# Optimization experiments

Measured on AMD Instinct MI355X. Metric: run time of the kernel, lower is better.

## Reference

```python
import jax, jax.numpy as jnp
from jax import lax
import numpy as np

B, C_IN, C_OUT, RN, H, W = 8, 64, 64, 4, 128, 128
DN = ('NCHW', 'OIHW', 'NCHW')
BN_EPS = 1e-5


def setup_inputs() -> dict:
    key = jax.random.key(0)
    k1, k2, k3, k4 = jax.random.split(key, 4)
    x = jax.random.normal(k1, (B, C_IN, H, W), dtype=jnp.float32)
    # per-sample, per-region dynamic 3x3 kernels (generated by a hypernet upstream)
    kernel = jax.random.normal(k2, (B, RN, C_OUT, C_IN, 3, 3), dtype=jnp.float32) * 0.05
    mask_w = jax.random.normal(k3, (RN, C_IN, 3, 3), dtype=jnp.float32) * 0.05
    mask_b = jax.random.normal(k4, (RN,), dtype=jnp.float32) * 0.01
    bn_gamma = jnp.ones((C_OUT,), dtype=jnp.float32)
    bn_beta = jnp.zeros((C_OUT,), dtype=jnp.float32)
    bn_mean = jnp.zeros((C_OUT,), dtype=jnp.float32)
    bn_var = jnp.ones((C_OUT,), dtype=jnp.float32)
    return {"x": x, "kernel": kernel, "mask_w": mask_w, "mask_b": mask_b,
            "bn_gamma": bn_gamma, "bn_beta": bn_beta,
            "bn_mean": bn_mean, "bn_var": bn_var}


def reference(x, kernel, mask_w, mask_b, bn_gamma, bn_beta, bn_mean, bn_var):
    b, c, h, w = x.shape
    rn, out_c = kernel.shape[1], kernel.shape[2]

    # region masks: 3x3 conv -> softmax over region axis (eval path of GumbelSoftmax2D)
    logits = lax.conv_general_dilated(x, mask_w, (1, 1), 'SAME', dimension_numbers=DN)
    logits = logits + mask_b[None, :, None, None]          # [b, RN, h, w]
    masks = jax.nn.softmax(logits, axis=1)

    # per-sample per-region dynamic conv as one grouped conv with b*RN groups
    xg = jnp.broadcast_to(x[:, None], (b, rn, c, h, w)).reshape(1, b * rn * c, h, w)
    kg = kernel.reshape(b * rn * out_c, c, 3, 3)
    y = lax.conv_general_dilated(xg, kg, (1, 1), 'SAME', dimension_numbers=DN,
                                 feature_group_count=b * rn)
    y = y.reshape(b, rn, out_c, h, w)

    # mask-weighted sum over regions
    y = jnp.sum(y * masks[:, :, None], axis=1)             # [b, out_c, h, w]

    # BatchNorm2d (eval: running stats) + ReLU
    inv = bn_gamma / jnp.sqrt(bn_var + BN_EPS)
    y = (y - bn_mean[None, :, None, None]) * inv[None, :, None, None] \
        + bn_beta[None, :, None, None]
    out = jax.nn.relu(y)
    return out, masks
```

## Files before the change

### kernel.cpp

```cpp
#include <hip/hip_runtime.h>
#include <hip/hip_bf16.h>

#define B_    8
#define CIN   64
#define COUT  64
#define RN_   4
#define H_    128
#define W_    128
#define HW_   (H_ * W_)
#define BN_EPS 1e-5f

typedef short v8s __attribute__((ext_vector_type(8)));
typedef float v4f __attribute__((ext_vector_type(4)));

__device__ __forceinline__ unsigned short f2bf(float f) {
    unsigned int u = __float_as_uint(f);
    u += 0x7FFFu + ((u >> 16) & 1u);
    return (unsigned short)(u >> 16);
}

__global__ __launch_bounds__(256) void prep(const float* __restrict__ x,
                                            const float* __restrict__ kr,
                                            unsigned short* __restrict__ xT,
                                            unsigned short* __restrict__ kT) {
    __shared__ float sl[16 * 64 * 9];
    if (blockIdx.x < 1024) {
        const int b = blockIdx.x >> 7, h = blockIdx.x & 127;
        const float* xp = x + (size_t)b * CIN * HW_ + (size_t)h * W_;
        for (int idx = threadIdx.x; idx < CIN * W_; idx += 256) {
            const int c = idx >> 7, w = idx & 127;
            sl[c * 129 + w] = xp[(size_t)c * HW_ + w];
        }
        __syncthreads();
        unsigned short* op = xT + ((size_t)b * H_ + h) * (W_ * CIN);
        for (int idx = threadIdx.x; idx < (W_ * CIN) / 8; idx += 256) {
            const int w = idx >> 3, c0 = (idx & 7) << 3;
            int4 v;
            v.x = f2bf(sl[(c0 + 0) * 129 + w]) | ((unsigned)f2bf(sl[(c0 + 1) * 129 + w]) << 16);
            v.y = f2bf(sl[(c0 + 2) * 129 + w]) | ((unsigned)f2bf(sl[(c0 + 3) * 129 + w]) << 16);
            v.z = f2bf(sl[(c0 + 4) * 129 + w]) | ((unsigned)f2bf(sl[(c0 + 5) * 129 + w]) << 16);
            v.w = f2bf(sl[(c0 + 6) * 129 + w]) | ((unsigned)f2bf(sl[(c0 + 7) * 129 + w]) << 16);
            *(int4*)(op + (w << 6) + c0) = v;
        }
    } else {
        const int bid = blockIdx.x - 1024;
        const int br = bid >> 2, oq = bid & 3;
        const float* src = kr + ((size_t)br * 64 + oq * 16) * (64 * 9);
        for (int idx = threadIdx.x; idx < 2304; idx += 256)
            *(float4*)&sl[idx << 2] = *(const float4*)&src[idx << 2];
        __syncthreads();
        unsigned short* dst = kT + (size_t)br * (9 * 4096) + oq * (16 * 64);
        for (int idx = threadIdx.x; idx < 1152; idx += 256) {
            const int t = idx >> 7, rem = idx & 127, o16 = rem >> 3, c8 = (rem & 7) << 3;
            unsigned short s[8];
            #pragma unroll
            for (int j = 0; j < 8; j++)
                s[j] = f2bf(sl[(o16 * 64 + c8 + j) * 9 + t]);
            int4 v;
            v.x = s[0] | ((unsigned)s[1] << 16);
            v.y = s[2] | ((unsigned)s[3] << 16);
            v.z = s[4] | ((unsigned)s[5] << 16);
            v.w = s[6] | ((unsigned)s[7] << 16);
            *(int4*)(dst + t * 4096 + o16 * 64 + c8) = v;
        }
    }
}

#define WPAD     72
#define XS_W     66
#define XS_ROWS  6
#define AS_ELEMS (COUT * WPAD)
#define XS_ELEMS (XS_ROWS * XS_W * WPAD)

__global__ __launch_bounds__(256, 2) void main_conv(
        const unsigned short* __restrict__ xT,
        const unsigned short* __restrict__ kT,
        const float* __restrict__ mw, const float* __restrict__ mb,
        const float* __restrict__ bn_gamma, const float* __restrict__ bn_beta,
        const float* __restrict__ bn_mean,  const float* __restrict__ bn_var,
        float* __restrict__ outp, float* __restrict__ masks_g) {
    __shared__ unsigned short xs[XS_ELEMS];
    __shared__ unsigned short as[2 * AS_ELEMS];
    __shared__ unsigned short mws[9 * 4 * 64];
    __shared__ float scale_s[COUT];
    __shared__ float shift_s[COUT];

    const int tid = threadIdx.x;
    const int b  = blockIdx.z;
    const int w0 = blockIdx.y << 6;
    const int h0 = blockIdx.x << 2;
    const int lane = tid & 63, wv = tid >> 6;
    const int i = lane & 15, g = lane >> 4;
    const int h_out = h0 + wv;

    const unsigned short* kb = kT + (size_t)b * (36 * 4096);
    int4 areg[2];
    #pragma unroll
    for (int q = 0; q < 2; q++)
        areg[q] = *(const int4*)(kb + ((q * 256 + tid) << 3));

    const unsigned short* xb = xT + (size_t)b * (HW_ * CIN);
    #pragma unroll
    for (int row = 0; row < XS_ROWS; row++) {
        const int h_in = h0 - 1 + row;
        const bool hok = (h_in >= 0) && (h_in < H_);
        for (int idx = tid; idx < XS_W * 8; idx += 256) {
            const int w = idx >> 3, c8 = (idx & 7) << 3;
            const int w_in = w0 - 1 + w;
            int4 v = make_int4(0, 0, 0, 0);
            if (hok && (w_in >= 0) && (w_in < W_))
                v = *(const int4*)(xb + ((h_in * W_ + w_in) << 6) + c8);
            *(int4*)(&xs[(row * XS_W + w) * WPAD + c8]) = v;
        }
    }
    for (int idx = tid; idx < 9 * 4 * 64; idx += 256) {
        const int t = idx >> 8, rc = idx & 255, r = rc >> 6, c = rc & 63;
        mws[(t << 8) + (r << 6) + c] = f2bf(mw[((r << 6) + c) * 9 + t]);
    }
    if (tid < COUT) {
        const float sc = bn_gamma[tid] * rsqrtf(bn_var[tid] + BN_EPS);
        scale_s[tid] = sc;
        shift_s[tid] = bn_beta[tid] - bn_mean[tid] * sc;
    }
    const float mb0 = mb[0], mb1 = mb[1], mb2 = mb[2], mb3 = mb[3];

    int bbase[4];
    #pragma unroll
    for (int fn = 0; fn < 4; fn++)
        bbase[fn] = ((wv + 1) * XS_W + fn * 16 + i + 1) * WPAD + g * 8;

    v4f y_acc[4][4], o_acc[4][4], lg_acc[4];
    #pragma unroll
    for (int fm = 0; fm < 4; fm++)
        #pragma unroll
        for (int fn = 0; fn < 4; fn++) {
            y_acc[fm][fn] = (v4f){0.f, 0.f, 0.f, 0.f};
            o_acc[fm][fn] = (v4f){0.f, 0.f, 0.f, 0.f};
        }
    #pragma unroll
    for (int fn = 0; fn < 4; fn++) lg_acc[fn] = (v4f){0.f, 0.f, 0.f, 0.f};

    unsigned mk0[4], mk1[4];

    int r = 0, tap = 0;
    for (int rt = 0; rt < 36; rt++) {
        const int buf = (rt & 1) * AS_ELEMS;
        #pragma unroll
        for (int q = 0; q < 2; q++) {
            const int c = q * 256 + tid;
            *(int4*)(&as[buf + (c >> 3) * WPAD + ((c & 7) << 3)]) = areg[q];
        }
        __syncthreads();
        if (rt < 35) {
            const unsigned short* kn = kb + ((rt + 1) << 12);
            #pragma unroll
            for (int q = 0; q < 2; q++)
                areg[q] = *(const int4*)(kn + ((q * 256 + tid) << 3));
        }
        const int toff = ((tap / 3) * XS_W + (tap % 3)) * WPAD - (XS_W + 1) * WPAD;
        const bool do_lg = (rt < 9);
        #pragma unroll
        for (int ks = 0; ks < 2; ks++) {
            v8s a[4], bfr[4];
            #pragma unroll
            for (int fm = 0; fm < 4; fm++)
                a[fm] = *(const v8s*)(&as[buf + (fm * 16 + i) * WPAD + ks * 32 + g * 8]);
            #pragma unroll
            for (int fn = 0; fn < 4; fn++)
                bfr[fn] = *(const v8s*)(&xs[bbase[fn] + toff + ks * 32]);
            if (do_lg) {
                const v8s am = *(const v8s*)(&mws[(tap << 8) + ((i & 3) << 6) + ks * 32 + g * 8]);
                #pragma unroll
                for (int fn = 0; fn < 4; fn++)
                    lg_acc[fn] = __builtin_amdgcn_mfma_f32_16x16x32_bf16(
                        am, bfr[fn], lg_acc[fn], 0, 0, 0);
            }
            #pragma unroll
            for (int fm = 0; fm < 4; fm++)
                #pragma unroll
                for (int fn = 0; fn < 4; fn++)
                    y_acc[fm][fn] = __builtin_amdgcn_mfma_f32_16x16x32_bf16(
                        a[fm], bfr[fn], y_acc[fm][fn], 0, 0, 0);
        }
        if (rt == 8) {
            #pragma unroll
            for (int fn = 0; fn < 4; fn++) {
                const float l0 = lg_acc[fn][0] + mb0, l1 = lg_acc[fn][1] + mb1;
                const float l2 = lg_acc[fn][2] + mb2, l3 = lg_acc[fn][3] + mb3;
                const float mx = fmaxf(fmaxf(l0, l1), fmaxf(l2, l3));
                const float e0 = __expf(l0 - mx), e1 = __expf(l1 - mx);
                const float e2 = __expf(l2 - mx), e3 = __expf(l3 - mx);
                const float inv = 1.f / (e0 + e1 + e2 + e3);
                const float m0 = e0 * inv, m1 = e1 * inv, m2 = e2 * inv, m3 = e3 * inv;
                if (g == 0) {
                    float* mp = masks_g + ((size_t)b * RN_ * H_ + h_out) * W_ + w0 + fn * 16 + i;
                    mp[0] = m0; mp[HW_] = m1; mp[2 * HW_] = m2; mp[3 * HW_] = m3;
                }
                mk0[fn] = f2bf(m0) | ((unsigned)f2bf(m1) << 16);
                mk1[fn] = f2bf(m2) | ((unsigned)f2bf(m3) << 16);
            }
        }
        if (++tap == 9) {
            tap = 0;
            #pragma unroll
            for (int fn = 0; fn < 4; fn++) {
                unsigned pk = (r & 2) ? mk1[fn] : mk0[fn];
                pk = __shfl(pk, i);
                const float mv = (r & 1) ? __uint_as_float(pk & 0xffff0000u)
                                         : __uint_as_float(pk << 16);
                #pragma unroll
                for (int fm = 0; fm < 4; fm++) {
                    o_acc[fm][fn] += mv * y_acc[fm][fn];
                    y_acc[fm][fn] = (v4f){0.f, 0.f, 0.f, 0.f};
                }
            }
            r++;
        }
    }

    #pragma unroll
    for (int fm = 0; fm < 4; fm++) {
        #pragma unroll
        for (int reg = 0; reg < 4; reg++) {
            const int o = fm * 16 + g * 4 + reg;
            const float sc = scale_s[o], sh = shift_s[o];
            float* rowp = outp + (((size_t)b * COUT + o) * H_ + h_out) * W_ + w0 + i;
            #pragma unroll
            for (int fn = 0; fn < 4; fn++) {
                const float v = o_acc[fm][fn][reg] * sc + sh;
                rowp[fn * 16] = fmaxf(v, 0.f);
            }
        }
    }
}

extern "C" void kernel_launch(void* const* d_in, const int* in_sizes, int n_in,
                              void* d_out, int out_size, void* d_ws, size_t ws_size,
                              hipStream_t stream) {
    const float* x     = (const float*)d_in[0];
    const float* kr    = (const float*)d_in[1];
    const float* mw    = (const float*)d_in[2];
    const float* mb    = (const float*)d_in[3];
    const float* gamma = (const float*)d_in[4];
    const float* beta  = (const float*)d_in[5];
    const float* mean  = (const float*)d_in[6];
    const float* var   = (const float*)d_in[7];

    float* outp  = (float*)d_out;
    float* masks = outp + (size_t)B_ * COUT * HW_;

    unsigned short* xT = (unsigned short*)d_ws;
    unsigned short* kT = xT + (size_t)B_ * HW_ * CIN;

    hipLaunchKernelGGL(prep, dim3(1152), dim3(256), 0, stream, x, kr, xT, kT);
    hipLaunchKernelGGL(main_conv, dim3(H_ / 4, 2, B_), dim3(256), 0, stream,
                       xT, kT, mw, mb, gamma, beta, mean, var, outp, masks);
}
```

Measured before the change: 156.5 us.

## Load dynamic-kernel A fragments directly from global into registers, unroll tap loop

Removes the shared-memory staging buffer for the per-sample weight tiles. Each lane now loads its MFMA A fragments straight from global memory into a double-buffered register array, which drops the per-step __syncthreads and the LDS writes and reads. The 36-step loop is fully unrolled with compile-time tap offsets. The cost is higher register pressure (16 v8s fragments) and redundant global loads across waves, since all four waves fetch the same weights.

```diff
diff --git a/kernel.cpp b/kernel.cpp
--- a/kernel.cpp
+++ b/kernel.cpp
@@ -69,7 +69,6 @@
 #define WPAD     72
 #define XS_W     66
 #define XS_ROWS  6
-#define AS_ELEMS (COUT * WPAD)
 #define XS_ELEMS (XS_ROWS * XS_W * WPAD)
 
 __global__ __launch_bounds__(256, 2) void main_conv(
@@ -80,7 +79,6 @@
         const float* __restrict__ bn_mean,  const float* __restrict__ bn_var,
         float* __restrict__ outp, float* __restrict__ masks_g) {
     __shared__ unsigned short xs[XS_ELEMS];
-    __shared__ unsigned short as[2 * AS_ELEMS];
     __shared__ unsigned short mws[9 * 4 * 64];
     __shared__ float scale_s[COUT];
     __shared__ float shift_s[COUT];
@@ -93,11 +91,12 @@
     const int i = lane & 15, g = lane >> 4;
     const int h_out = h0 + wv;
 
-    const unsigned short* kb = kT + (size_t)b * (36 * 4096);
-    int4 areg[2];
-    #pragma unroll
-    for (int q = 0; q < 2; q++)
-        areg[q] = *(const int4*)(kb + ((q * 256 + tid) << 3));
+    const unsigned short* ka = kT + (size_t)b * (36 * 4096) + (i << 6) + (g << 3);
+
+    v8s ab[2][8];
+    #pragma unroll
+    for (int f = 0; f < 8; f++)
+        ab[0][f] = *(const v8s*)(ka + ((f >> 1) << 10) + ((f & 1) << 5));
 
     const unsigned short* xb = xT + (size_t)b * (HW_ * CIN);
     #pragma unroll
@@ -127,7 +126,7 @@
     int bbase[4];
     #pragma unroll
     for (int fn = 0; fn < 4; fn++)
-        bbase[fn] = ((wv + 1) * XS_W + fn * 16 + i + 1) * WPAD + g * 8;
+        bbase[fn] = (wv * XS_W + fn * 16 + i) * WPAD + g * 8;
 
     v4f y_acc[4][4], o_acc[4][4], lg_acc[4];
     #pragma unroll
@@ -142,81 +141,83 @@
 
     unsigned mk0[4], mk1[4];
 
-    int r = 0, tap = 0;
-    for (int rt = 0; rt < 36; rt++) {
-        const int buf = (rt & 1) * AS_ELEMS;
-        #pragma unroll
-        for (int q = 0; q < 2; q++) {
-            const int c = q * 256 + tid;
-            *(int4*)(&as[buf + (c >> 3) * WPAD + ((c & 7) << 3)]) = areg[q];
-        }
-        __syncthreads();
-        if (rt < 35) {
-            const unsigned short* kn = kb + ((rt + 1) << 12);
+    auto do_softmax = [&]() {
+        #pragma unroll
+        for (int fn = 0; fn < 4; fn++) {
+            const float l0 = lg_acc[fn][0] + mb0, l1 = lg_acc[fn][1] + mb1;
+            const float l2 = lg_acc[fn][2] + mb2, l3 = lg_acc[fn][3] + mb3;
+            const float mx = fmaxf(fmaxf(l0, l1), fmaxf(l2, l3));
+            const float e0 = __expf(l0 - mx), e1 = __expf(l1 - mx);
+            const float e2 = __expf(l2 - mx), e3 = __expf(l3 - mx);
+            const float inv = 1.f / (e0 + e1 + e2 + e3);
+            const float m0 = e0 * inv, m1 = e1 * inv, m2 = e2 * inv, m3 = e3 * inv;
+            if (g == 0) {
+                float* mp = masks_g + ((size_t)b * RN_ * H_ + h_out) * W_ + w0 + fn * 16 + i;
+                mp[0] = m0; mp[HW_] = m1; mp[2 * HW_] = m2; mp[3 * HW_] = m3;
+            }
+            mk0[fn] = f2bf(m0) | ((unsigned)f2bf(m1) << 16);
+            mk1[fn] = f2bf(m2) | ((unsigned)f2bf(m3) << 16);
+        }
+    };
+    auto fold_region = [&](int r) {
+        #pragma unroll
+        for (int fn = 0; fn < 4; fn++) {
+            unsigned pk = (r & 2) ? mk1[fn] : mk0[fn];
+            pk = __shfl(pk, i);
+            const float mv = (r & 1) ? __uint_as_float(pk & 0xffff0000u)
+                                     : __uint_as_float(pk << 16);
             #pragma unroll
-            for (int q = 0; q < 2; q++)
-                areg[q] = *(const int4*)(kn + ((q * 256 + tid) << 3));
-        }
-        const int toff = ((tap / 3) * XS_W + (tap % 3)) * WPAD - (XS_W + 1) * WPAD;
-        const bool do_lg = (rt < 9);
-        #pragma unroll
-        for (int ks = 0; ks < 2; ks++) {
-            v8s a[4], bfr[4];
-            #pragma unroll
-            for (int fm = 0; fm < 4; fm++)
-                a[fm] = *(const v8s*)(&as[buf + (fm * 16 + i) * WPAD + ks * 32 + g * 8]);
-            #pragma unroll
-            for (int fn = 0; fn < 4; fn++)
-                bfr[fn] = *(const v8s*)(&xs[bbase[fn] + toff + ks * 32]);
-            if (do_lg) {
-                const v8s am = *(const v8s*)(&mws[(tap << 8) + ((i & 3) << 6) + ks * 32 + g * 8]);
-                #pragma unroll
-                for (int fn = 0; fn < 4; fn++)
-                    lg_acc[fn] = __builtin_amdgcn_mfma_f32_16x16x32_bf16(
-                        am, bfr[fn], lg_acc[fn], 0, 0, 0);
+            for (int fm = 0; fm < 4; fm++) {
+                o_acc[fm][fn] += mv * y_acc[fm][fn];
+                y_acc[fm][fn] = (v4f){0.f, 0.f, 0.f, 0.f};
             }
-            #pragma unroll
-            for (int fm = 0; fm < 4; fm++)
-                #pragma unroll
-                for (int fn = 0; fn < 4; fn++)
-                    y_acc[fm][fn] = __builtin_amdgcn_mfma_f32_16x16x32_bf16(
-                        a[fm], bfr[fn], y_acc[fm][fn], 0, 0, 0);
-        }
-        if (rt == 8) {
-            #pragma unroll
-            for (int fn = 0; fn < 4; fn++) {
-                const float l0 = lg_acc[fn][0] + mb0, l1 = lg_acc[fn][1] + mb1;
-                const float l2 = lg_acc[fn][2] + mb2, l3 = lg_acc[fn][3] + mb3;
-                const float mx = fmaxf(fmaxf(l0, l1), fmaxf(l2, l3));
-                const float e0 = __expf(l0 - mx), e1 = __expf(l1 - mx);
-                const float e2 = __expf(l2 - mx), e3 = __expf(l3 - mx);
-                const float inv = 1.f / (e0 + e1 + e2 + e3);
-                const float m0 = e0 * inv, m1 = e1 * inv, m2 = e2 * inv, m3 = e3 * inv;
-                if (g == 0) {
-                    float* mp = masks_g + ((size_t)b * RN_ * H_ + h_out) * W_ + w0 + fn * 16 + i;
-                    mp[0] = m0; mp[HW_] = m1; mp[2 * HW_] = m2; mp[3 * HW_] = m3;
-                }
-                mk0[fn] = f2bf(m0) | ((unsigned)f2bf(m1) << 16);
-                mk1[fn] = f2bf(m2) | ((unsigned)f2bf(m3) << 16);
-            }
-        }
-        if (++tap == 9) {
-            tap = 0;
-            #pragma unroll
-            for (int fn = 0; fn < 4; fn++) {
-                unsigned pk = (r & 2) ? mk1[fn] : mk0[fn];
-                pk = __shfl(pk, i);
-                const float mv = (r & 1) ? __uint_as_float(pk & 0xffff0000u)
-                                         : __uint_as_float(pk << 16);
-                #pragma unroll
-                for (int fm = 0; fm < 4; fm++) {
-                    o_acc[fm][fn] += mv * y_acc[fm][fn];
-                    y_acc[fm][fn] = (v4f){0.f, 0.f, 0.f, 0.f};
-                }
-            }
-            r++;
-        }
-    }
+        }
+    };
+
+    __syncthreads();
+
+#define RT_STEP(RT)                                                              \
+    {                                                                            \
+        constexpr int cur = (RT) & 1, nxt = cur ^ 1;                             \
+        if ((RT) < 35) {                                                         \
+            const unsigned short* kn = ka + (((RT) + 1) << 12);                  \
+            _Pragma("unroll")                                                    \
+            for (int f = 0; f < 8; f++)                                          \
+                ab[nxt][f] = *(const v8s*)(kn + ((f >> 1) << 10) + ((f & 1) << 5)); \
+        }                                                                        \
+        constexpr int tap = (RT) % 9;                                            \
+        constexpr int toff = ((tap / 3) * XS_W + (tap % 3)) * WPAD;              \
+        _Pragma("unroll")                                                        \
+        for (int ks = 0; ks < 2; ks++) {                                         \
+            v8s bfr[4];                                                          \
+            _Pragma("unroll")                                                    \
+            for (int fn = 0; fn < 4; fn++)                                       \
+                bfr[fn] = *(const v8s*)(&xs[bbase[fn] + toff + ks * 32]);        \
+            if ((RT) < 9) {                                                      \
+                const v8s am = *(const v8s*)(&mws[(tap << 8) + ((i & 3) << 6) + ks * 32 + g * 8]); \
+                _Pragma("unroll")                                                \
+                for (int fn = 0; fn < 4; fn++)                                   \
+                    lg_acc[fn] = __builtin_amdgcn_mfma_f32_16x16x32_bf16(        \
+                        am, bfr[fn], lg_acc[fn], 0, 0, 0);                       \
+            }                                                                    \
+            _Pragma("unroll")                                                    \
+            for (int fm = 0; fm < 4; fm++)                                       \
+                _Pragma("unroll")                                                \
+                for (int fn = 0; fn < 4; fn++)                                   \
+                    y_acc[fm][fn] = __builtin_amdgcn_mfma_f32_16x16x32_bf16(     \
+                        ab[cur][fm * 2 + ks], bfr[fn], y_acc[fm][fn], 0, 0, 0);  \
+        }                                                                        \
+        if ((RT) == 8) do_softmax();                                             \
+        if (tap == 8) fold_region((RT) / 9);                                     \
+    }
+
+    RT_STEP(0)  RT_STEP(1)  RT_STEP(2)  RT_STEP(3)  RT_STEP(4)  RT_STEP(5)
+    RT_STEP(6)  RT_STEP(7)  RT_STEP(8)  RT_STEP(9)  RT_STEP(10) RT_STEP(11)
+    RT_STEP(12) RT_STEP(13) RT_STEP(14) RT_STEP(15) RT_STEP(16) RT_STEP(17)
+    RT_STEP(18) RT_STEP(19) RT_STEP(20) RT_STEP(21) RT_STEP(22) RT_STEP(23)
+    RT_STEP(24) RT_STEP(25) RT_STEP(26) RT_STEP(27) RT_STEP(28) RT_STEP(29)
+    RT_STEP(30) RT_STEP(31) RT_STEP(32) RT_STEP(33) RT_STEP(34) RT_STEP(35)
+#undef RT_STEP
 
     #pragma unroll
     for (int fm = 0; fm < 4; fm++) {
```

Result: slower. 196.1 us (+25.3%).
